# Optimization experiments

Hardware: AMD Instinct MI355X
Metric: run time of the kernel (lower is better)

The kernel has to match this reference:

```python
import jax, jax.numpy as jnp
import numpy as np

N = 50000      # n_nodes
E = 800000     # n_edges
IN_NF = 64     # in_node_nf
HID = 128      # hidden_nf
OUT_NF = 64    # out_node_nf
L = 4          # n_layers
EH = HID // 2  # edge MLP hidden width (edge_nf_ratio=2)
C = 1.0        # aggregation scaling constant


def _w(k, shape):
    # fan-in scaled init (matches nn.Linear scale roughly)
    return jax.random.normal(k, shape, dtype=jnp.float32) / np.sqrt(shape[-2]).astype(np.float32)


def setup_inputs() -> dict:
    key = jax.random.key(0)
    ks = jax.random.split(key, 10)
    h = jax.random.normal(ks[0], (N, IN_NF), dtype=jnp.float32)
    edges = jax.random.randint(ks[1], (2, E), 0, N, dtype=jnp.int32)
    return {
        "h": h,
        "edges": edges,
        "W_in": _w(ks[2], (IN_NF, HID)),
        "b_in": jnp.zeros((HID,), jnp.float32),
        # stacked per-layer GCL params, leading dim L
        "eW1": _w(ks[3], (L, 2 * HID, EH)),
        "eb1": jnp.zeros((L, EH), jnp.float32),
        "eW2": _w(ks[4], (L, EH, EH)),
        "eb2": jnp.zeros((L, EH), jnp.float32),
        "nW1": _w(ks[5], (L, HID + EH, HID)),
        "nb1": jnp.zeros((L, HID), jnp.float32),
        "nW2": _w(ks[6], (L, HID, HID)),
        "nb2": jnp.zeros((L, HID), jnp.float32),
        "W_out": _w(ks[7], (HID, OUT_NF)),
        "b_out": jnp.zeros((OUT_NF,), jnp.float32),
    }


def reference(h, edges, W_in, b_in, eW1, eb1, eW2, eb2, nW1, nb1, nW2, nb2, W_out, b_out):
    row, col = edges[0], edges[1]
    h = h @ W_in + b_in  # [N, HID] embedding_in

    def layer(hc, p):
        w1, b1, w2, b2, m1, c1, m2, c2 = p
        # edge model: gather endpoints, concat, 2-layer SiLU MLP
        m = jnp.concatenate([hc[row], hc[col]], axis=1)          # [E, 2*HID]
        m = jax.nn.silu(m @ w1 + b1)                             # [E, EH]
        m = jax.nn.silu(m @ w2 + b2)                             # [E, EH]
        # node model: scatter-sum messages to source nodes, scale by C
        agg = jax.ops.segment_sum(m, row, num_segments=N) * C    # [N, EH]
        z = jnp.concatenate([hc, agg], axis=1)                   # [N, HID+EH]
        z = jax.nn.silu(z @ m1 + c1)
        z = z @ m2 + c2                                          # [N, HID]
        return hc + z, None  # residual=True

    h, _ = jax.lax.scan(layer, h, (eW1, eb1, eW2, eb2, nW1, nb1, nW2, nb2))
    return h @ W_out + b_out  # [N, OUT_NF] embedding_out
```

## Files before the change

kernel.cpp:

```cpp
#include <hip/hip_runtime.h>
#include <hip/hip_bf16.h>
#include <hip/hip_fp16.h>
#include <cstdint>
#include <cstddef>

#define N_NODES 50000
#define N_EDGES 800000
#define NBKT    196
#define BSH     8
#define BCHUNK  2048
#define CAP     6144

typedef __attribute__((ext_vector_type(8))) short short8;
typedef __attribute__((ext_vector_type(4))) float floatx4;
typedef __attribute__((ext_vector_type(2))) float floatx2;
typedef __attribute__((ext_vector_type(4))) unsigned int uintx4;
typedef __attribute__((ext_vector_type(2))) unsigned int uintx2;
typedef __attribute__((ext_vector_type(8))) _Float16 half8v;

__device__ inline float bf2f(unsigned short u) {
    union { unsigned int i; float f; } v; v.i = ((unsigned int)u) << 16; return v.f;
}
__device__ inline unsigned short f2bf(float f) {
    union { float f; unsigned int i; } v; v.f = f;
    unsigned int u = v.i;
    return (unsigned short)((u + 0x7FFFu + ((u >> 16) & 1u)) >> 16);
}
__device__ inline unsigned int f2bf_pk(float a, float b) {
    __hip_bfloat162 h2 = __float22bfloat162_rn(make_float2(a, b));
    return *reinterpret_cast<unsigned int*>(&h2);
}
__device__ inline unsigned short f2fh(float f) {
    _Float16 h = (_Float16)f;
    return __builtin_bit_cast(unsigned short, h);
}
__device__ inline unsigned int f2fh_pk(float a, float b) {
    typedef __attribute__((ext_vector_type(2))) __fp16 h2v;
    h2v r = __builtin_amdgcn_cvt_pkrtz(a, b);
    return __builtin_bit_cast(unsigned int, r);
}
__device__ inline __half2 u2h(unsigned int u) { return __builtin_bit_cast(__half2, u); }
__device__ inline unsigned int h2u(__half2 h) { return __builtin_bit_cast(unsigned int, h); }
__device__ inline __half2 silu_h2(__half2 x) {
    const __half2 nlog2e = __float2half2_rn(-1.4426950408889634f);
    const __half2 one    = __float2half2_rn(1.0f);
    __half2 e = h2exp2(__hmul2(x, nlog2e));
    return __hmul2(x, h2rcp(__hadd2(e, one)));
}
__device__ inline float silu_f(float x) {
    float e = __expf(-x);
    return x * __builtin_amdgcn_rcpf(1.0f + e);
}

__device__ inline int block_excl_scan_256(int v, int* buf) {
    int tid = threadIdx.x;
    buf[tid] = v;
    __syncthreads();
    #pragma unroll
    for (int off = 1; off < 256; off <<= 1) {
        int t = (tid >= off) ? buf[tid - off] : 0;
        __syncthreads();
        buf[tid] += t;
        __syncthreads();
    }
    return buf[tid] - v;
}

__device__ inline void pack_std(const float* __restrict__ src,
                                unsigned short* __restrict__ dst,
                                int NOUT, long j) {
    int i = (int)(j & 7);
    long rest = j >> 3;
    int n = (int)(rest % NOUT);
    int kb = (int)(rest / NOUT);
    dst[j] = f2bf(src[(long)(kb * 8 + i) * NOUT + n]);
}
__device__ inline void pack_std_h(const float* __restrict__ src,
                                  unsigned short* __restrict__ dst,
                                  int NOUT, long j) {
    int i = (int)(j & 7);
    long rest = j >> 3;
    int n = (int)(rest % NOUT);
    int kb = (int)(rest / NOUT);
    dst[j] = f2fh(src[(long)(kb * 8 + i) * NOUT + n]);
}

#define SW_IN 8192L
#define SW_OUT 8192L
#define SW1   16384L
#define SE2   4096L
#define SN1   24576L
#define SN2   16384L
#define SB    128L
#define PERL  (SW1 + SE2 + SN1 + SN2 + SB)
#define PACK_TOTAL (SW_IN + SW_OUT + 4 * PERL)
#define PACK_GRID_TOTAL (PACK_TOTAL + NBKT)

__global__ __launch_bounds__(256) void pack_kernel(
    const float* __restrict__ W_in,
    const float* __restrict__ W_out, const float* __restrict__ eW1,
    const float* __restrict__ eb1, const float* __restrict__ eW2,
    const float* __restrict__ nW1, const float* __restrict__ nW2,
    unsigned short* __restrict__ Winp,
    unsigned short* __restrict__ Woutp, unsigned short* __restrict__ W1p,
    unsigned short* __restrict__ eW2p, unsigned short* __restrict__ nW1p,
    unsigned short* __restrict__ nW2p, float* __restrict__ biasP,
    int* __restrict__ bucketCursor)
{
    long idx = (long)blockIdx.x * 256 + threadIdx.x;
    if (idx >= PACK_TOTAL) {
        long t = idx - PACK_TOTAL;
        if (t < NBKT) bucketCursor[t] = 0;
        return;
    }
    long j = idx;
    if (j < SW_IN) { pack_std(W_in, Winp, 128, j); return; }
    j -= SW_IN;
    if (j < SW_OUT) { pack_std(W_out, Woutp, 64, j); return; }
    j -= SW_OUT;
    int l = (int)(j / PERL);
    long r = j % PERL;
    if (r < SW1) {
        int i = (int)(r & 7);
        int n = (int)((r >> 3) & 127);
        int kb = (int)(r >> 10);
        int k = kb * 8 + i;
        const float* w = eW1 + (long)l * 256 * 64;
        float v = (n < 64) ? w[(long)k * 64 + n] : w[(long)(128 + k) * 64 + (n - 64)];
        W1p[(long)l * SW1 + r] = f2bf(v);
        return;
    }
    r -= SW1;
    if (r < SE2) { pack_std_h(eW2 + (long)l * 4096, eW2p + (long)l * SE2, 64, r); return; }
    r -= SE2;
    if (r < SN1) { pack_std(nW1 + (long)l * 24576, nW1p + (long)l * SN1, 128, r); return; }
    r -= SN1;
    if (r < SN2) { pack_std(nW2 + (long)l * 16384, nW2p + (long)l * SN2, 128, r); return; }
    r -= SN2;
    biasP[(long)l * 128 + r] = (r < 64) ? eb1[(long)l * 64 + r] : 0.0f;
}

#define SROWE 264
#define BE_SMEM_BYTES (64 * SROWE * 2)

__global__ __launch_bounds__(256) void bin_embed_k(
    const int* __restrict__ erow, const int* __restrict__ ecol,
    int* __restrict__ bucketCursor,
    int2* __restrict__ binned, int E, int binGrid,
    const float* __restrict__ h0, const unsigned short* __restrict__ Win,
    const float* __restrict__ b_in, const unsigned short* __restrict__ W1,
    const float* __restrict__ biasP,
    unsigned short* __restrict__ hB, unsigned short* __restrict__ Pout,
    float* __restrict__ aggZ, int M)
{
    __shared__ char SMEM[BE_SMEM_BYTES];
    const int tid = threadIdx.x;

    if (blockIdx.x < binGrid) {
        int* cnt      = (int*)SMEM;
        int* binStart = cnt + NBKT;
        int* gbase    = binStart + NBKT;
        int* scanbuf  = gbase + NBKT;
        int2* staged  = (int2*)(scanbuf + 256);

        const int base = blockIdx.x * BCHUNK;
        const int nloc = min(BCHUNK, E - base);

        for (int i = tid; i < NBKT; i += 256) cnt[i] = 0;
        __syncthreads();

        int2 ed[BCHUNK / 256];
        int  bo[BCHUNK / 256];
        #pragma unroll
        for (int i = 0; i < BCHUNK / 256; i++) {
            int jl = i * 256 + tid;
            if (jl < nloc) {
                int j = base + jl;
                int r = erow[j], c = ecol[j];
                ed[i] = make_int2(r, c);
                int b = r >> BSH;
                int off = atomicAdd(&cnt[b], 1);
                bo[i] = (b << 12) | off;
            } else bo[i] = -1;
        }
        __syncthreads();

        int v = (tid < NBKT) ? cnt[tid] : 0;
        int excl = block_excl_scan_256(v, scanbuf);
        if (tid < NBKT) binStart[tid] = excl;
        if (tid < NBKT && v > 0)
            gbase[tid] = atomicAdd(&bucketCursor[tid], v);
        __syncthreads();

        #pragma unroll
        for (int i = 0; i < BCHUNK / 256; i++) {
            if (bo[i] >= 0)
                staged[binStart[bo[i] >> 12] + (bo[i] & 0xFFF)] = ed[i];
        }
        __syncthreads();

        for (int j = tid; j < nloc; j += 256) {
            int2 e = staged[j];
            int b = e.x >> BSH;
            int off = gbase[b] + (j - binStart[b]);
            if (off < CAP)
                binned[(size_t)b * CAP + off] = e;
        }
        return;
    }

    unsigned short* S = (unsigned short*)SMEM;
    const int m0 = (blockIdx.x - binGrid) * 64;
    const int wave = tid >> 6;
    const int lane = tid & 63;
    const int lrow = lane & 15;
    const int quad = lane >> 4;
    const int elb = wave * 16 + quad * 4;

    for (int t = tid; t < 64 * 16; t += 256) {
        int rr = t >> 4, c = t & 15;
        int row = m0 + rr;
        floatx4 v = {0, 0, 0, 0};
        if (row < M) v = *(const floatx4*)(h0 + (size_t)row * 64 + c * 4);
        uintx2 u = { f2bf_pk(v[0], v[1]), f2bf_pk(v[2], v[3]) };
        *(uintx2*)(&S[rr * SROWE + c * 4]) = u;
    }
    __syncthreads();

    {
        floatx4 z = {0, 0, 0, 0};
        for (int t = tid; t < 64 * 16; t += 256) {
            int rr = t >> 4, c = t & 15;
            int row = m0 + rr;
            if (row < M) *(floatx4*)(aggZ + (size_t)row * 64 + c * 4) = z;
        }
    }

    const unsigned short* arow = &S[(wave * 16 + lrow) * SROWE];

    floatx4 acc[8];
    #pragma unroll
    for (int i = 0; i < 8; i++) acc[i] = (floatx4){0, 0, 0, 0};
    #pragma unroll
    for (int kt = 0; kt < 2; kt++) {
        short8 afrag = *(const short8*)(arow + kt * 32 + quad * 8);
        int kb = kt * 4 + quad;
        #pragma unroll
        for (int nt = 0; nt < 8; nt++) {
            short8 bfrag = *(const short8*)(Win + (size_t)(kb * 128 + nt * 16 + lrow) * 8);
            acc[nt] = __builtin_amdgcn_mfma_f32_16x16x32_bf16(afrag, bfrag, acc[nt], 0, 0, 0);
        }
    }

    #pragma unroll
    for (int nt = 0; nt < 8; nt++) {
        int n = nt * 16 + lrow;
        float bv = b_in[n];
        floatx4 v4;
        #pragma unroll
        for (int r = 0; r < 4; r++) v4[r] = acc[nt][r] + bv;
        unsigned int p01 = f2bf_pk(v4[0], v4[1]);
        unsigned int p23 = f2bf_pk(v4[2], v4[3]);
        S[(elb + 0) * SROWE + n] = (unsigned short)(p01 & 0xFFFF);
        S[(elb + 1) * SROWE + n] = (unsigned short)(p01 >> 16);
        S[(elb + 2) * SROWE + n] = (unsigned short)(p23 & 0xFFFF);
        S[(elb + 3) * SROWE + n] = (unsigned short)(p23 >> 16);
    }

    floatx4 acc3[8];
    #pragma unroll
    for (int i = 0; i < 8; i++) acc3[i] = (floatx4){0, 0, 0, 0};
    #pragma unroll
    for (int kt = 0; kt < 4; kt++) {
        short8 afrag = *(const short8*)(arow + kt * 32 + quad * 8);
        int kb = kt * 4 + quad;
        #pragma unroll
        for (int nt = 0; nt < 8; nt++) {
            short8 bfrag = *(const short8*)(W1 + (size_t)(kb * 128 + nt * 16 + lrow) * 8);
            acc3[nt] = __builtin_amdgcn_mfma_f32_16x16x32_bf16(afrag, bfrag, acc3[nt], 0, 0, 0);
        }
    }
    #pragma unroll
    for (int nt = 0; nt < 8; nt++) {
        int n = nt * 16 + lrow;
        float bv = biasP[n];
        unsigned int p01 = f2fh_pk(acc3[nt][0] + bv, acc3[nt][1] + bv);
        unsigned int p23 = f2fh_pk(acc3[nt][2] + bv, acc3[nt][3] + bv);
        S[(elb + 0) * SROWE + 128 + n] = (unsigned short)(p01 & 0xFFFF);
        S[(elb + 1) * SROWE + 128 + n] = (unsigned short)(p01 >> 16);
        S[(elb + 2) * SROWE + 128 + n] = (unsigned short)(p23 & 0xFFFF);
        S[(elb + 3) * SROWE + 128 + n] = (unsigned short)(p23 >> 16);
    }
    __syncthreads();

    for (int t = tid; t < 64 * 32; t += 256) {
        int rr = t / 32, c = t % 32;
        int row = m0 + rr;
        if (row < M) {
            if (c < 16)
                *(uintx4*)(hB + (size_t)row * 128 + c * 8) =
                    *(const uintx4*)(&S[rr * SROWE + c * 8]);
            else
                *(uintx4*)(Pout + (size_t)row * 128 + (c - 16) * 8) =
                    *(const uintx4*)(&S[rr * SROWE + 128 + (c - 16) * 8]);
        }
    }
}

__global__ __launch_bounds__(256) void sort_k(
    const int2* __restrict__ binned, const int* __restrict__ bucketCursor,
    int2* __restrict__ eidx, unsigned long long* __restrict__ zmask)
{
    __shared__ int2 st[CAP];
    __shared__ int cnt[256];
    __shared__ int cur[256];
    __shared__ int scanbuf[256];
    __shared__ int baseS[2];
    const int b = blockIdx.x;
    const int tid = threadIdx.x;

    {
        int v = (tid < NBKT) ? min(bucketCursor[tid], CAP) : 0;
        int excl = block_excl_scan_256(v, scanbuf);
        if (tid == b) { baseS[0] = excl; baseS[1] = excl + v; }
    }
    __syncthreads();
    const int s0 = baseS[0];
    const int n = baseS[1] - s0;

    cnt[tid] = 0;
    __syncthreads();
    const int2* bsrc = binned + (size_t)b * CAP;
    for (int j = tid; j < n; j += 256) {
        int2 e = bsrc[j];
        st[j] = e;
        atomicAdd(&cnt[e.x & 255], 1);
    }
    __syncthreads();
    int myCnt = cnt[tid];
    int excl = block_excl_scan_256(myCnt, scanbuf);
    cur[tid] = excl;
    const int myLo = s0 + excl;
    __syncthreads();
    for (int j = tid; j < n; j += 256) {
        int2 e = st[j];
        int pos = atomicAdd(&cur[e.x & 255], 1);
        eidx[s0 + pos] = e;
    }

    {
        bool nz;
        if (myCnt == 0) nz = true;
        else {
            int lo = myLo, hi = myLo + myCnt;
            int A = lo >> 6, Bk = (hi - 1) >> 6;
            nz = (Bk > A) || ((lo & 63) == 0) || (((hi - 1) & 63) == 63);
        }
        unsigned long long m = __ballot(nz);
        if ((tid & 63) == 0)
            zmask[(((size_t)b << 8) + tid) >> 6] = m;
    }
}

__global__ __launch_bounds__(256) void edge_fused_k(
    const int2* __restrict__ eidx,
    const unsigned short* __restrict__ P,
    const unsigned short* __restrict__ Bp,
    const float* __restrict__ b2, float* __restrict__ agg, int E)
{
    __shared__ float M2s[64 * 68];
    __shared__ int ridS[64];
    __shared__ short segStartS[66];
    __shared__ int nsegS;
    const int tid = threadIdx.x;
    const int wave = tid >> 6;
    const int lane = tid & 63;
    const int lrow = lane & 15;
    const int quad = lane >> 4;
    const int e0 = blockIdx.x * 64;
    const int el = wave * 16 + lrow;
    const int e = e0 + el;

    floatx4 acc[4];
    #pragma unroll
    for (int nt = 0; nt < 4; nt++) {
        float bv = b2[nt * 16 + lrow];
        acc[nt] = (floatx4){bv, bv, bv, bv};
    }

    half8v af0 = {};
    half8v af1 = {};
    if (e < E) {
        int2 rc = eidx[e];
        int rr = rc.x, cc = rc.y;
        if (quad == 0) ridS[el] = rr;
        const uintx4* pt = (const uintx4*)(P + (size_t)rr * 128 + quad * 8);
        const uintx4* pb = (const uintx4*)(P + (size_t)cc * 128 + 64 + quad * 8);
        uintx4 t0 = pt[0], t1 = pt[4];
        uintx4 b0 = pb[0], b1 = pb[4];
        uintx4 O0, O1;
        #pragma unroll
        for (int i = 0; i < 4; i++) {
            O0[i] = h2u(silu_h2(__hadd2(u2h(t0[i]), u2h(b0[i]))));
            O1[i] = h2u(silu_h2(__hadd2(u2h(t1[i]), u2h(b1[i]))));
        }
        af0 = __builtin_bit_cast(half8v, O0);
        af1 = __builtin_bit_cast(half8v, O1);
    } else if (quad == 0) {
        ridS[el] = -1;
    }

    #pragma unroll
    for (int nt = 0; nt < 4; nt++) {
        half8v bf0 = *(const half8v*)(Bp + (size_t)((0 * 4 + quad) * 64 + nt * 16 + lrow) * 8);
        acc[nt] = __builtin_amdgcn_mfma_f32_16x16x32_f16(af0, bf0, acc[nt], 0, 0, 0);
        half8v bf1 = *(const half8v*)(Bp + (size_t)((1 * 4 + quad) * 64 + nt * 16 + lrow) * 8);
        acc[nt] = __builtin_amdgcn_mfma_f32_16x16x32_f16(af1, bf1, acc[nt], 0, 0, 0);
    }

    #pragma unroll
    for (int nt = 0; nt < 4; nt++) {
        int n = nt * 16 + lrow;
        #pragma unroll
        for (int r = 0; r < 4; r++) {
            int el2 = wave * 16 + quad * 4 + r;
            M2s[el2 * 68 + n] = silu_f(acc[nt][r]);
        }
    }
    __syncthreads();

    if (tid < 64) {
        bool st = (ridS[tid] >= 0) && (tid == 0 || ridS[tid] != ridS[tid - 1]);
        unsigned long long m = __ballot(st);
        if (st) {
            int pos = __popcll(m & ((1ull << tid) - 1));
            segStartS[pos] = (short)tid;
        }
        if (tid == 0) {
            int ns = __popcll(m);
            nsegS = ns;
            int nvalid = E - e0;
            if (nvalid > 64) nvalid = 64;
            segStartS[ns] = (short)nvalid;
        }
    }
    __syncthreads();

    {
        int f = tid & 63;
        int g = tid >> 6;
        int ns = nsegS;
        for (int j = g; j < ns; j += 4) {
            int a = segStartS[j], b = segStartS[j + 1];
            float s = 0.0f;
            for (int el2 = a; el2 < b; el2++) s += M2s[el2 * 68 + f];
            int rv = ridS[a];
            if (j == 0 || j == ns - 1)
                atomicAdd(&agg[(size_t)rv * 64 + f], s);
            else
                agg[(size_t)rv * 64 + f] = s;
        }
    }
}

#define SROW 264
template<int FINAL>
__global__ __launch_bounds__(256) void node_fused_k(
    const unsigned short* __restrict__ hbf, const float* __restrict__ agg,
    const unsigned short* __restrict__ W1, const float* __restrict__ b1,
    const unsigned short* __restrict__ W2, const float* __restrict__ b2,
    const unsigned short* __restrict__ B3, const float* __restrict__ bias3,
    unsigned short* __restrict__ hB, unsigned short* __restrict__ Pout,
    float* __restrict__ outF, float* __restrict__ aggZ,
    const unsigned long long* __restrict__ zmask, int M)
{
    __shared__ unsigned short S[32 * SROW];
    const int tid = threadIdx.x;
    const int m0 = blockIdx.x * 32;
    const int wave = tid >> 6;
    const int lane = tid & 63;
    const int lrow = lane & 15;
    const int quad = lane >> 4;
    const int g = wave >> 1;
    const int h = wave & 1;
    const int elb = g * 16 + quad * 4;

    short8 afa0, afa1;
    {
        const float* ap = agg + (size_t)(m0 + g * 16 + lrow) * 64;
        floatx4 q0 = *(const floatx4*)(ap + quad * 8);
        floatx4 q1 = *(const floatx4*)(ap + quad * 8 + 4);
        floatx4 q2 = *(const floatx4*)(ap + 32 + quad * 8);
        floatx4 q3 = *(const floatx4*)(ap + 32 + quad * 8 + 4);
        unsigned int c0[4] = { f2bf_pk(q0[0], q0[1]), f2bf_pk(q0[2], q0[3]),
                               f2bf_pk(q1[0], q1[1]), f2bf_pk(q1[2], q1[3]) };
        unsigned int c1[4] = { f2bf_pk(q2[0], q2[1]), f2bf_pk(q2[2], q2[3]),
                               f2bf_pk(q3[0], q3[1]), f2bf_pk(q3[2], q3[3]) };
        afa0 = *(const short8*)c0;
        afa1 = *(const short8*)c1;
    }

    for (int t = tid; t < 32 * 16; t += 256) {
        int rr = t >> 4, c = t & 15;
        int row = m0 + rr;
        uintx4 val = {0, 0, 0, 0};
        if (row < M) val = *(const uintx4*)(hbf + (size_t)row * 128 + c * 8);
        *(uintx4*)(&S[rr * SROW + c * 8]) = val;
    }
    __syncthreads();

    if (!FINAL) {
        unsigned long long zm = zmask[m0 >> 6];
        int bb = m0 & 63;
        floatx4 z = {0, 0, 0, 0};
        for (int t = tid; t < 32 * 16; t += 256) {
            int rr = t >> 4, c = t & 15;
            int row = m0 + rr;
            if (row < M && ((zm >> (bb + rr)) & 1ull))
                *(floatx4*)(aggZ + (size_t)row * 64 + c * 4) = z;
        }
    }

    const unsigned short* arow = &S[(g * 16 + lrow) * SROW];

    floatx4 acc[4];
    #pragma unroll
    for (int i = 0; i < 4; i++) acc[i] = (floatx4){0, 0, 0, 0};
    #pragma unroll
    for (int kt = 0; kt < 4; kt++) {
        short8 afrag = *(const short8*)(arow + kt * 32 + quad * 8);
        int kb = kt * 4 + quad;
        #pragma unroll
        for (int j = 0; j < 4; j++) {
            int n = (4 * h + j) * 16 + lrow;
            short8 bfrag = *(const short8*)(W1 + (size_t)(kb * 128 + n) * 8);
            acc[j] = __builtin_amdgcn_mfma_f32_16x16x32_bf16(afrag, bfrag, acc[j], 0, 0, 0);
        }
    }
    #pragma unroll
    for (int j = 0; j < 4; j++) {
        int n = (4 * h + j) * 16 + lrow;
        short8 b4 = *(const short8*)(W1 + (size_t)((16 + quad) * 128 + n) * 8);
        acc[j] = __builtin_amdgcn_mfma_f32_16x16x32_bf16(afa0, b4, acc[j], 0, 0, 0);
        short8 b5 = *(const short8*)(W1 + (size_t)((20 + quad) * 128 + n) * 8);
        acc[j] = __builtin_amdgcn_mfma_f32_16x16x32_bf16(afa1, b5, acc[j], 0, 0, 0);
    }

    #pragma unroll
    for (int j = 0; j < 4; j++) {
        int n = (4 * h + j) * 16 + lrow;
        float bv = b1[n];
        unsigned int p01 = f2bf_pk(silu_f(acc[j][0] + bv), silu_f(acc[j][1] + bv));
        unsigned int p23 = f2bf_pk(silu_f(acc[j][2] + bv), silu_f(acc[j][3] + bv));
        S[(elb + 0) * SROW + 128 + n] = (unsigned short)(p01 & 0xFFFF);
        S[(elb + 1) * SROW + 128 + n] = (unsigned short)(p01 >> 16);
        S[(elb + 2) * SROW + 128 + n] = (unsigned short)(p23 & 0xFFFF);
        S[(elb + 3) * SROW + 128 + n] = (unsigned short)(p23 >> 16);
    }
    __syncthreads();

    floatx4 acc2[4];
    #pragma unroll
    for (int i = 0; i < 4; i++) acc2[i] = (floatx4){0, 0, 0, 0};
    #pragma unroll
    for (int kt = 0; kt < 4; kt++) {
        short8 afrag = *(const short8*)(arow + 128 + kt * 32 + quad * 8);
        int kb = kt * 4 + quad;
        #pragma unroll
        for (int j = 0; j < 4; j++) {
            int n = (4 * h + j) * 16 + lrow;
            short8 bfrag = *(const short8*)(W2 + (size_t)(kb * 128 + n) * 8);
            acc2[j] = __builtin_amdgcn_mfma_f32_16x16x32_bf16(afrag, bfrag, acc2[j], 0, 0, 0);
        }
    }

    #pragma unroll
    for (int j = 0; j < 4; j++) {
        int n = (4 * h + j) * 16 + lrow;
        float bv = b2[n];
        floatx4 v4;
        #pragma unroll
        for (int r = 0; r < 4; r++) {
            float res = bf2f(S[(elb + r) * SROW + n]);
            v4[r] = acc2[j][r] + bv + res;
        }
        unsigned int p01 = f2bf_pk(v4[0], v4[1]);
        unsigned int p23 = f2bf_pk(v4[2], v4[3]);
        S[(elb + 0) * SROW + n] = (unsigned short)(p01 & 0xFFFF);
        S[(elb + 1) * SROW + n] = (unsigned short)(p01 >> 16);
        S[(elb + 2) * SROW + n] = (unsigned short)(p23 & 0xFFFF);
        S[(elb + 3) * SROW + n] = (unsigned short)(p23 >> 16);
    }
    __syncthreads();

    constexpr int NT3 = FINAL ? 2 : 4;
    constexpr int NO3 = FINAL ? 64 : 128;
    floatx4 acc3[NT3];
    #pragma unroll
    for (int i = 0; i < NT3; i++) acc3[i] = (floatx4){0, 0, 0, 0};
    #pragma unroll
    for (int kt = 0; kt < 4; kt++) {
        short8 afrag = *(const short8*)(arow + kt * 32 + quad * 8);
        int kb = kt * 4 + quad;
        #pragma unroll
        for (int j = 0; j < NT3; j++) {
            int n = (NT3 * h + j) * 16 + lrow;
            short8 bfrag = *(const short8*)(B3 + (size_t)(kb * NO3 + n) * 8);
            acc3[j] = __builtin_amdgcn_mfma_f32_16x16x32_bf16(afrag, bfrag, acc3[j], 0, 0, 0);
        }
    }
    #pragma unroll
    for (int j = 0; j < NT3; j++) {
        int n = (NT3 * h + j) * 16 + lrow;
        float bv = bias3[n];
        if (FINAL) {
            #pragma unroll
            for (int r = 0; r < 4; r++)
                ((float*)(&S[(elb + r) * SROW + 128]))[n] = acc3[j][r] + bv;
        } else {
            unsigned int p01 = f2fh_pk(acc3[j][0] + bv, acc3[j][1] + bv);
            unsigned int p23 = f2fh_pk(acc3[j][2] + bv, acc3[j][3] + bv);
            S[(elb + 0) * SROW + 128 + n] = (unsigned short)(p01 & 0xFFFF);
            S[(elb + 1) * SROW + 128 + n] = (unsigned short)(p01 >> 16);
            S[(elb + 2) * SROW + 128 + n] = (unsigned short)(p23 & 0xFFFF);
            S[(elb + 3) * SROW + 128 + n] = (unsigned short)(p23 >> 16);
        }
    }
    __syncthreads();

    if (FINAL) {
        for (int t = tid; t < 32 * 16; t += 256) {
            int rr = t >> 4, c = t & 15;
            int row = m0 + rr;
            if (row < M)
                *(floatx4*)(outF + (size_t)row * 64 + c * 4) =
                    *(const floatx4*)((const float*)(&S[rr * SROW + 128]) + c * 4);
        }
    } else {
        for (int t = tid; t < 32 * 32; t += 256) {
            int rr = t >> 5, c = t & 31;
            int row = m0 + rr;
            if (row < M) {
                if (c < 16)
                    *(uintx4*)(hB + (size_t)row * 128 + c * 8) =
                        *(const uintx4*)(&S[rr * SROW + c * 8]);
                else
                    *(uintx4*)(Pout + (size_t)row * 128 + (c - 16) * 8) =
                        *(const uintx4*)(&S[rr * SROW + 128 + (c - 16) * 8]);
            }
        }
    }
}

extern "C" void kernel_launch(void* const* d_in, const int* in_sizes, int n_in,
                              void* d_out, int out_size, void* d_ws, size_t ws_size,
                              hipStream_t stream) {
    const float* h0   = (const float*)d_in[0];
    const int*   edges= (const int*)d_in[1];
    const float* W_in = (const float*)d_in[2];
    const float* b_in = (const float*)d_in[3];
    const float* eW1  = (const float*)d_in[4];
    const float* eb1  = (const float*)d_in[5];
    const float* eW2  = (const float*)d_in[6];
    const float* eb2  = (const float*)d_in[7];
    const float* nW1  = (const float*)d_in[8];
    const float* nb1  = (const float*)d_in[9];
    const float* nW2  = (const float*)d_in[10];
    const float* nb2  = (const float*)d_in[11];
    const float* W_out= (const float*)d_in[12];
    const float* b_out= (const float*)d_in[13];
    float* out = (float*)d_out;

    const int E = in_sizes[1] / 2;
    const int* erow = edges;
    const int* ecol = edges + E;

    char* ws = (char*)d_ws;
    unsigned short* hbf  = (unsigned short*)(ws + 0);
    int2*           binned=(int2*)(ws + 12800000);
    unsigned short* P    = (unsigned short*)(ws + 38424576);
    float*          agg  = (float*)(ws + 51224576);
    int2*           eidx = (int2*)(ws + 76824576);
    float*          biasP= (float*)(ws + 83224576);
    unsigned short* Winp = (unsigned short*)(ws + 83226624);
    unsigned short* Woutp= (unsigned short*)(ws + 83243008);
    unsigned short* W1p  = (unsigned short*)(ws + 83259392);
    unsigned short* eW2p = (unsigned short*)(ws + 83390464);
    unsigned short* nW1p = (unsigned short*)(ws + 83423232);
    unsigned short* nW2p = (unsigned short*)(ws + 83619840);
    int*            bucketCursor=(int*)(ws + 83752960);
    unsigned long long* zmask = (unsigned long long*)(ws + 83754496);

    const int gemm_grid = (N_NODES + 63) / 64;
    const int node_grid = (N_NODES + 31) / 32;
    const int edge_grid = (E + 63) / 64;
    const int pack_grid = (int)((PACK_GRID_TOTAL + 255) / 256);
    const int bin_grid  = (E + BCHUNK - 1) / BCHUNK;

    pack_kernel<<<pack_grid, 256, 0, stream>>>(W_in, W_out, eW1, eb1, eW2,
                                               nW1, nW2, Winp, Woutp, W1p,
                                               eW2p, nW1p, nW2p, biasP,
                                               bucketCursor);

    bin_embed_k<<<bin_grid + gemm_grid, 256, 0, stream>>>(
        erow, ecol, bucketCursor, binned, E, bin_grid,
        h0, Winp, b_in, W1p, biasP, hbf, P, agg, N_NODES);

    sort_k<<<NBKT, 256, 0, stream>>>(binned, bucketCursor, eidx, zmask);

    for (int l = 0; l < 4; l++) {
        edge_fused_k<<<edge_grid, 256, 0, stream>>>(
            eidx, P, eW2p + (size_t)l * SE2, eb2 + (size_t)l * 64, agg, E);
        if (l < 3) {
            node_fused_k<0><<<node_grid, 256, 0, stream>>>(
                hbf, agg, nW1p + (size_t)l * SN1, nb1 + (size_t)l * 128,
                nW2p + (size_t)l * SN2, nb2 + (size_t)l * 128,
                W1p + (size_t)(l + 1) * SW1, biasP + (size_t)(l + 1) * 128,
                hbf, P, nullptr, agg, zmask, N_NODES);
        } else {
            node_fused_k<1><<<node_grid, 256, 0, stream>>>(
                hbf, agg, nW1p + (size_t)l * SN1, nb1 + (size_t)l * 128,
                nW2p + (size_t)l * SN2, nb2 + (size_t)l * 128,
                Woutp, b_out, nullptr, nullptr, out, nullptr, zmask, N_NODES);
        }
    }
}
```

Baseline: 372.3 us.

## Regroup preprocessing kernels: fuse binning with weight packing and sort with embedding

```diff
diff --git a/kernel.cpp b/kernel.cpp
--- a/kernel.cpp
+++ b/kernel.cpp
@@ -94,25 +94,81 @@
 #define SB    128L
 #define PERL  (SW1 + SE2 + SN1 + SN2 + SB)
 #define PACK_TOTAL (SW_IN + SW_OUT + 4 * PERL)
-#define PACK_GRID_TOTAL (PACK_TOTAL + NBKT)
-
-__global__ __launch_bounds__(256) void pack_kernel(
-    const float* __restrict__ W_in,
-    const float* __restrict__ W_out, const float* __restrict__ eW1,
-    const float* __restrict__ eb1, const float* __restrict__ eW2,
-    const float* __restrict__ nW1, const float* __restrict__ nW2,
-    unsigned short* __restrict__ Winp,
-    unsigned short* __restrict__ Woutp, unsigned short* __restrict__ W1p,
-    unsigned short* __restrict__ eW2p, unsigned short* __restrict__ nW1p,
-    unsigned short* __restrict__ nW2p, float* __restrict__ biasP,
-    int* __restrict__ bucketCursor)
+#define PACK_BLOCKS ((int)((PACK_TOTAL + 255) / 256))
+
+#define PB_SMEM_BYTES (NBKT * 3 * 4 + 256 * 4 + BCHUNK * 8)
+
+__global__ __launch_bounds__(256) void bin_pack_k(
+    const int* __restrict__ erow, const int* __restrict__ ecol,
+    int* __restrict__ bucketCursor, int2* __restrict__ binned,
+    int E, int binGrid,
+    const float* __restrict__ W_in, const float* __restrict__ W_out,
+    const float* __restrict__ eW1, const float* __restrict__ eb1,
+    const float* __restrict__ eW2, const float* __restrict__ nW1,
+    const float* __restrict__ nW2,
+    unsigned short* __restrict__ Winp, unsigned short* __restrict__ Woutp,
+    unsigned short* __restrict__ W1p, unsigned short* __restrict__ eW2p,
+    unsigned short* __restrict__ nW1p, unsigned short* __restrict__ nW2p,
+    float* __restrict__ biasP)
 {
-    long idx = (long)blockIdx.x * 256 + threadIdx.x;
-    if (idx >= PACK_TOTAL) {
-        long t = idx - PACK_TOTAL;
-        if (t < NBKT) bucketCursor[t] = 0;
+    __shared__ char SMEM[PB_SMEM_BYTES];
+    const int tid = threadIdx.x;
+
+    if (blockIdx.x < binGrid) {
+        int* cnt      = (int*)SMEM;
+        int* binStart = cnt + NBKT;
+        int* gbase    = binStart + NBKT;
+        int* scanbuf  = gbase + NBKT;
+        int2* staged  = (int2*)(scanbuf + 256);
+
+        const int base = blockIdx.x * BCHUNK;
+        const int nloc = min(BCHUNK, E - base);
+
+        for (int i = tid; i < NBKT; i += 256) cnt[i] = 0;
+        __syncthreads();
+
+        int2 ed[BCHUNK / 256];
+        int  bo[BCHUNK / 256];
+        #pragma unroll
+        for (int i = 0; i < BCHUNK / 256; i++) {
+            int jl = i * 256 + tid;
+            if (jl < nloc) {
+                int j = base + jl;
+                int r = erow[j], c = ecol[j];
+                ed[i] = make_int2(r, c);
+                int b = r >> BSH;
+                int off = atomicAdd(&cnt[b], 1);
+                bo[i] = (b << 12) | off;
+            } else bo[i] = -1;
+        }
+        __syncthreads();
+
+        int v = (tid < NBKT) ? cnt[tid] : 0;
+        int excl = block_excl_scan_256(v, scanbuf);
+        if (tid < NBKT) binStart[tid] = excl;
+        if (tid < NBKT && v > 0)
+            gbase[tid] = atomicAdd(&bucketCursor[tid], v);
+        __syncthreads();
+
+        #pragma unroll
+        for (int i = 0; i < BCHUNK / 256; i++) {
+            if (bo[i] >= 0)
+                staged[binStart[bo[i] >> 12] + (bo[i] & 0xFFF)] = ed[i];
+        }
+        __syncthreads();
+
+        for (int j = tid; j < nloc; j += 256) {
+            int2 e = staged[j];
+            int b = e.x >> BSH;
+            int off = gbase[b] + (j - binStart[b]);
+            if (off < CAP)
+                binned[(size_t)b * CAP + off] = e;
+        }
         return;
     }
+
+    long idx = (long)(blockIdx.x - binGrid) * 256 + tid;
+    if (idx >= PACK_TOTAL) return;
     long j = idx;
     if (j < SW_IN) { pack_std(W_in, Winp, 128, j); return; }
     j -= SW_IN;
@@ -141,76 +197,70 @@
 }
 
 #define SROWE 264
-#define BE_SMEM_BYTES (64 * SROWE * 2)
-
-__global__ __launch_bounds__(256) void bin_embed_k(
-    const int* __restrict__ erow, const int* __restrict__ ecol,
-    int* __restrict__ bucketCursor,
-    int2* __restrict__ binned, int E, int binGrid,
+#define SE_SMEM_BYTES (64 * SROWE * 2)
+
+__global__ __launch_bounds__(256) void sort_embed_k(
+    const int2* __restrict__ binned, const int* __restrict__ bucketCursor,
+    int2* __restrict__ eidx, unsigned long long* __restrict__ zmask,
     const float* __restrict__ h0, const unsigned short* __restrict__ Win,
     const float* __restrict__ b_in, const unsigned short* __restrict__ W1,
     const float* __restrict__ biasP,
     unsigned short* __restrict__ hB, unsigned short* __restrict__ Pout,
     float* __restrict__ aggZ, int M)
 {
-    __shared__ char SMEM[BE_SMEM_BYTES];
+    __shared__ char SMEM[SE_SMEM_BYTES];
     const int tid = threadIdx.x;
 
-    if (blockIdx.x < binGrid) {
-        int* cnt      = (int*)SMEM;
-        int* binStart = cnt + NBKT;
-        int* gbase    = binStart + NBKT;
-        int* scanbuf  = gbase + NBKT;
-        int2* staged  = (int2*)(scanbuf + 256);
-
-        const int base = blockIdx.x * BCHUNK;
-        const int nloc = min(BCHUNK, E - base);
-
-        for (int i = tid; i < NBKT; i += 256) cnt[i] = 0;
-        __syncthreads();
-
-        int2 ed[BCHUNK / 256];
-        int  bo[BCHUNK / 256];
-        #pragma unroll
-        for (int i = 0; i < BCHUNK / 256; i++) {
-            int jl = i * 256 + tid;
-            if (jl < nloc) {
-                int j = base + jl;
-                int r = erow[j], c = ecol[j];
-                ed[i] = make_int2(r, c);
-                int b = r >> BSH;
-                int off = atomicAdd(&cnt[b], 1);
-                bo[i] = (b << 12) | off;
-            } else bo[i] = -1;
-        }
-        __syncthreads();
-
-        int v = (tid < NBKT) ? cnt[tid] : 0;
-        int excl = block_excl_scan_256(v, scanbuf);
-        if (tid < NBKT) binStart[tid] = excl;
-        if (tid < NBKT && v > 0)
-            gbase[tid] = atomicAdd(&bucketCursor[tid], v);
-        __syncthreads();
-
-        #pragma unroll
-        for (int i = 0; i < BCHUNK / 256; i++) {
-            if (bo[i] >= 0)
-                staged[binStart[bo[i] >> 12] + (bo[i] & 0xFFF)] = ed[i];
-        }
-        __syncthreads();
-
-        for (int j = tid; j < nloc; j += 256) {
-            int2 e = staged[j];
-            int b = e.x >> BSH;
-            int off = gbase[b] + (j - binStart[b]);
-            if (off < CAP)
-                binned[(size_t)b * CAP + off] = e;
+    if (blockIdx.x < NBKT) {
+        int* cnt     = (int*)SMEM;
+        int* cur     = cnt + 256;
+        int* scanbuf = cur + 256;
+        int* baseS   = scanbuf + 256;
+        const int b = blockIdx.x;
+
+        {
+            int v = (tid < NBKT) ? min(bucketCursor[tid], CAP) : 0;
+            int excl = block_excl_scan_256(v, scanbuf);
+            if (tid == b) { baseS[0] = excl; baseS[1] = excl + v; }
+        }
+        __syncthreads();
+        const int s0 = baseS[0];
+        const int n = baseS[1] - s0;
+
+        cnt[tid] = 0;
+        __syncthreads();
+        const int2* bsrc = binned + (size_t)b * CAP;
+        for (int j = tid; j < n; j += 256)
+            atomicAdd(&cnt[bsrc[j].x & 255], 1);
+        __syncthreads();
+        int myCnt = cnt[tid];
+        int excl = block_excl_scan_256(myCnt, scanbuf);
+        cur[tid] = excl;
+        const int myLo = s0 + excl;
+        __syncthreads();
+        for (int j = tid; j < n; j += 256) {
+            int2 e = bsrc[j];
+            int pos = atomicAdd(&cur[e.x & 255], 1);
+            eidx[s0 + pos] = e;
+        }
+
+        {
+            bool nz;
+            if (myCnt == 0) nz = true;
+            else {
+                int lo = myLo, hi = myLo + myCnt;
+                int A = lo >> 6, Bk = (hi - 1) >> 6;
+                nz = (Bk > A) || ((lo & 63) == 0) || (((hi - 1) & 63) == 63);
+            }
+            unsigned long long m = __ballot(nz);
+            if ((tid & 63) == 0)
+                zmask[(((size_t)b << 8) + tid) >> 6] = m;
         }
         return;
     }
 
     unsigned short* S = (unsigned short*)SMEM;
-    const int m0 = (blockIdx.x - binGrid) * 64;
+    const int m0 = (blockIdx.x - NBKT) * 64;
     const int wave = tid >> 6;
     const int lane = tid & 63;
     const int lrow = lane & 15;
@@ -304,61 +354,6 @@
                 *(uintx4*)(Pout + (size_t)row * 128 + (c - 16) * 8) =
                     *(const uintx4*)(&S[rr * SROWE + 128 + (c - 16) * 8]);
         }
-    }
-}
-
-__global__ __launch_bounds__(256) void sort_k(
-    const int2* __restrict__ binned, const int* __restrict__ bucketCursor,
-    int2* __restrict__ eidx, unsigned long long* __restrict__ zmask)
-{
-    __shared__ int2 st[CAP];
-    __shared__ int cnt[256];
-    __shared__ int cur[256];
-    __shared__ int scanbuf[256];
-    __shared__ int baseS[2];
-    const int b = blockIdx.x;
-    const int tid = threadIdx.x;
-
-    {
-        int v = (tid < NBKT) ? min(bucketCursor[tid], CAP) : 0;
-        int excl = block_excl_scan_256(v, scanbuf);
-        if (tid == b) { baseS[0] = excl; baseS[1] = excl + v; }
-    }
-    __syncthreads();
-    const int s0 = baseS[0];
-    const int n = baseS[1] - s0;
-
-    cnt[tid] = 0;
-    __syncthreads();
-    const int2* bsrc = binned + (size_t)b * CAP;
-    for (int j = tid; j < n; j += 256) {
-        int2 e = bsrc[j];
-        st[j] = e;
-        atomicAdd(&cnt[e.x & 255], 1);
-    }
-    __syncthreads();
-    int myCnt = cnt[tid];
-    int excl = block_excl_scan_256(myCnt, scanbuf);
-    cur[tid] = excl;
-    const int myLo = s0 + excl;
-    __syncthreads();
-    for (int j = tid; j < n; j += 256) {
-        int2 e = st[j];
-        int pos = atomicAdd(&cur[e.x & 255], 1);
-        eidx[s0 + pos] = e;
-    }
-
-    {
-        bool nz;
-        if (myCnt == 0) nz = true;
-        else {
-            int lo = myLo, hi = myLo + myCnt;
-            int A = lo >> 6, Bk = (hi - 1) >> 6;
-            nz = (Bk > A) || ((lo & 63) == 0) || (((hi - 1) & 63) == 63);
-        }
-        unsigned long long m = __ballot(nz);
-        if ((tid & 63) == 0)
-            zmask[(((size_t)b << 8) + tid) >> 6] = m;
     }
 }
 
@@ -694,19 +689,18 @@
     const int gemm_grid = (N_NODES + 63) / 64;
     const int node_grid = (N_NODES + 31) / 32;
     const int edge_grid = (E + 63) / 64;
-    const int pack_grid = (int)((PACK_GRID_TOTAL + 255) / 256);
     const int bin_grid  = (E + BCHUNK - 1) / BCHUNK;
 
-    pack_kernel<<<pack_grid, 256, 0, stream>>>(W_in, W_out, eW1, eb1, eW2,
-                                               nW1, nW2, Winp, Woutp, W1p,
-                                               eW2p, nW1p, nW2p, biasP,
-                                               bucketCursor);
-
-    bin_embed_k<<<bin_grid + gemm_grid, 256, 0, stream>>>(
+    hipMemsetAsync(bucketCursor, 0, NBKT * 4, stream);
+
+    bin_pack_k<<<bin_grid + PACK_BLOCKS, 256, 0, stream>>>(
         erow, ecol, bucketCursor, binned, E, bin_grid,
+        W_in, W_out, eW1, eb1, eW2, nW1, nW2,
+        Winp, Woutp, W1p, eW2p, nW1p, nW2p, biasP);
+
+    sort_embed_k<<<NBKT + gemm_grid, 256, 0, stream>>>(
+        binned, bucketCursor, eidx, zmask,
         h0, Winp, b_in, W1p, biasP, hbf, P, agg, N_NODES);
-
-    sort_k<<<NBKT, 256, 0, stream>>>(binned, bucketCursor, eidx, zmask);
 
     for (int l = 0; l < 4; l++) {
         edge_fused_k<<<edge_grid, 256, 0, stream>>>(
```

New measurement: 367.2 us. Within noise of the previous version (-1.4%).
